# Kernel tuning notes

Measured on AMD Instinct MI355X. Metric: run time of the kernel, lower is better.

## Reference

```python
import jax, jax.numpy as jnp
import numpy as np

B, IN, N, W, R, U, OUT = 512, 128, 256, 64, 4, 256, 128
IFACE = R * W + 3 * W + 5 * R + 3  # 471
CLIP = 20.0
EPS = 1e-6


def setup_inputs() -> dict:
    key = jax.random.key(0)
    ks = jax.random.split(key, 20)
    return {
        'inputs': jax.random.normal(ks[0], (B, IN), jnp.float32),
        'M': jax.random.normal(ks[1], (B, N, W), jnp.float32),
        'usage': jax.random.uniform(ks[2], (B, N), jnp.float32),
        'link': jax.random.uniform(ks[3], (B, N, N), jnp.float32) * 0.01,
        'precedence': jax.random.uniform(ks[4], (B, N), jnp.float32) * 0.01,
        'ww_prev': jax.random.uniform(ks[5], (B, N), jnp.float32) / N,
        'wr_prev': jax.random.uniform(ks[6], (B, N, R), jnp.float32) / N,
        'h_prev': jax.random.normal(ks[7], (B, U), jnp.float32),
        'c_prev': jax.random.normal(ks[8], (B, U), jnp.float32),
        'rv_prev': jax.random.normal(ks[9], (B, W, R), jnp.float32),
        'Wk': jax.random.normal(ks[10], (IN + W * R, 4 * U), jnp.float32) * 0.05,
        'Wr': jax.random.normal(ks[11], (U, 4 * U), jnp.float32) * 0.05,
        'b_lstm': jnp.full((4 * U,), 0.1, jnp.float32),
        'Wi': jax.random.normal(ks[12], (U, IFACE), jnp.float32) * 0.05,
        'bi': jnp.full((IFACE,), 0.1, jnp.float32),
        'Wo': jax.random.normal(ks[13], (U + W * R, OUT), jnp.float32) * 0.05,
        'bo': jnp.zeros((OUT,), jnp.float32),
    }


def _parse_interface(v):
    sizes = [R * W, R, W, 1, W, W, R, 1, 1, 3 * R]
    offs = np.cumsum([0] + sizes)
    s = [v[:, offs[i]:offs[i + 1]] for i in range(len(sizes))]
    read_keys = s[0].reshape(-1, W, R)
    read_strengths = 1.0 + jax.nn.softplus(s[1])                 # [B,R]
    write_key = s[2].reshape(-1, W)                              # [B,W]
    write_strength = 1.0 + jax.nn.softplus(s[3])                 # [B,1]
    erase = jax.nn.sigmoid(s[4])                                 # [B,W]
    write_vec = s[5]                                             # [B,W]
    free_gates = jax.nn.sigmoid(s[6])                            # [B,R]
    alloc_gate = jax.nn.sigmoid(s[7])                            # [B,1]
    write_gate = jax.nn.sigmoid(s[8])                            # [B,1]
    read_modes = jax.nn.softmax(s[9].reshape(-1, 3, R), axis=1)  # [B,3,R]
    return (read_keys, read_strengths, write_key, write_strength, erase,
            write_vec, free_gates, alloc_gate, write_gate, read_modes)


def _forward(inputs, M, usage, link, precedence, ww_prev, wr_prev,
             h_prev, c_prev, rv_prev, Wk, Wr, b_lstm, Wi, bi, Wo, bo):
    # --- controller (keras LSTMCell: gate order i,f,c,o) ---
    x = jnp.concatenate([inputs, rv_prev.reshape(-1, W * R)], axis=1)
    z = x @ Wk + h_prev @ Wr + b_lstm
    zi, zf, zc, zo = jnp.split(z, 4, axis=1)
    c = jax.nn.sigmoid(zf) * c_prev + jax.nn.sigmoid(zi) * jnp.tanh(zc)
    h = jax.nn.sigmoid(zo) * jnp.tanh(c)
    h = jnp.clip(h, -CLIP, CLIP)
    # --- interface ---
    (read_keys, read_strengths, write_key, write_strength, erase,
     write_vec, free_gates, alloc_gate, write_gate, read_modes) = _parse_interface(h @ Wi + bi)
    # --- usage / retention ---
    psi = jnp.prod(1.0 - free_gates[:, None, :] * wr_prev, axis=2)     # [B,N]
    u = (usage + ww_prev - usage * ww_prev) * psi                      # [B,N]
    # --- allocation (sorted cumprod) ---
    idx = jnp.argsort(u, axis=1)                                        # ascending
    u_sorted = jnp.take_along_axis(u, idx, axis=1)
    cp = jnp.cumprod(u_sorted, axis=1)
    cp_excl = jnp.concatenate([jnp.ones_like(cp[:, :1]), cp[:, :-1]], axis=1)
    a_sorted = (1.0 - u_sorted) * cp_excl
    inv = jnp.argsort(idx, axis=1)
    alloc = jnp.take_along_axis(a_sorted, inv, axis=1)                  # [B,N]
    # --- write content addressing (cosine) ---
    Mn = jnp.linalg.norm(M, axis=2)                                     # [B,N]
    kw_n = jnp.linalg.norm(write_key, axis=1, keepdims=True)            # [B,1]
    sim_w = jnp.einsum('bnw,bw->bn', M, write_key) / (Mn * kw_n + EPS)
    cw = jax.nn.softmax(write_strength * sim_w, axis=1)                 # [B,N]
    ww = write_gate * (alloc_gate * alloc + (1.0 - alloc_gate) * cw)    # [B,N]
    # --- memory write ---
    M_new = M * (1.0 - ww[:, :, None] * erase[:, None, :]) + ww[:, :, None] * write_vec[:, None, :]
    # --- temporal link / precedence ---
    L_new = (1.0 - ww[:, :, None] - ww[:, None, :]) * link + ww[:, :, None] * precedence[:, None, :]
    L_new = L_new * (1.0 - jnp.eye(N, dtype=L_new.dtype))
    p_new = (1.0 - jnp.sum(ww, axis=1, keepdims=True)) * precedence + ww
    # --- read content addressing ---
    Mn2 = jnp.linalg.norm(M_new, axis=2)                                # [B,N]
    kr_n = jnp.linalg.norm(read_keys, axis=1)                           # [B,R]
    sim_r = jnp.einsum('bnw,bwr->bnr', M_new, read_keys) / (Mn2[:, :, None] * kr_n[:, None, :] + EPS)
    cr = jax.nn.softmax(read_strengths[:, None, :] * sim_r, axis=1)     # [B,N,R]
    # --- forward / backward weightings ---
    fwd = jnp.einsum('bnm,bmr->bnr', L_new, wr_prev)
    bwd = jnp.einsum('bmn,bmr->bnr', L_new, wr_prev)
    wr = (read_modes[:, 0, :][:, None, :] * bwd
          + read_modes[:, 1, :][:, None, :] * cr
          + read_modes[:, 2, :][:, None, :] * fwd)                      # [B,N,R]
    read_vectors = jnp.einsum('bnw,bnr->bwr', M_new, wr)                # [B,W,R]
    # --- final output ---
    final = jnp.concatenate([h, read_vectors.reshape(-1, W * R)], axis=1) @ Wo + bo
    return jnp.clip(final, -CLIP, CLIP)


def reference(inputs, M, usage, link, precedence, ww_prev, wr_prev,
              h_prev, c_prev, rv_prev, Wk, Wr, b_lstm, Wi, bi, Wo, bo):
    return _forward(inputs, M, usage, link, precedence, ww_prev, wr_prev,
                    h_prev, c_prev, rv_prev, Wk, Wr, b_lstm, Wi, bi, Wo, bo)
```

## Files before the change

### kernel.cpp

```cpp
#include <hip/hip_runtime.h>
#include <math.h>

#define Bsz 512
#define INsz 128
#define Nn 256
#define Ww 64
#define Rr 4
#define Uu 256
#define OUTsz 128
#define IFACEsz 471
#define XDIM 384
#define KL 640
#define G4 1024

__device__ __forceinline__ float sigf(float x){ return 1.0f/(1.0f+expf(-x)); }
__device__ __forceinline__ float softplusf_(float x){ return fmaxf(x,0.0f) + log1pf(expf(-fabsf(x))); }
__device__ __forceinline__ float4 f4fma(float s, float4 a, float4 acc){
  acc.x += s*a.x; acc.y += s*a.y; acc.z += s*a.z; acc.w += s*a.w; return acc;
}
__device__ __forceinline__ float4 f4add(float4 a, float4 b){
  a.x+=b.x; a.y+=b.y; a.z+=b.z; a.w+=b.w; return a;
}
__device__ __forceinline__ float4 f4max(float4 a, float4 b){
  a.x=fmaxf(a.x,b.x); a.y=fmaxf(a.y,b.y); a.z=fmaxf(a.z,b.z); a.w=fmaxf(a.w,b.w); return a;
}

__global__ __launch_bounds__(256) void k_packWi(
  const float* __restrict__ Wi, float* __restrict__ Wip)
{
  const int k = blockIdx.x, t = threadIdx.x;
  const int j2 = t + 256;
  Wip[(size_t)k*512 + t]  = Wi[(size_t)k*IFACEsz + t];
  Wip[(size_t)k*512 + j2] = (j2 < IFACEsz) ? Wi[(size_t)k*IFACEsz + j2] : 0.0f;
}

__global__ __launch_bounds__(512) void k_lstm(
  const float* __restrict__ inputs, const float* __restrict__ rvp,
  const float* __restrict__ hp, const float* __restrict__ Wk,
  const float* __restrict__ Wr, const float* __restrict__ bl,
  const float* __restrict__ cprev, float* __restrict__ h_out)
{
  const int t = threadIdx.x;
  const int tx = t & 7;
  const int tg = (t >> 3) & 3;
  const int tb = t >> 5;
  const int b0 = blockIdx.x * 16;
  const int cg = blockIdx.y * 32;
  const int col = tg*256 + cg + tx*4;
  __shared__ float Xs[16][68];
  __shared__ float zs[16][4][36];
  float4 acc = {0,0,0,0};
  for (int kc = 0; kc < KL; kc += 64){
    if (t < 256){
      const int rr = t >> 4, cc = (t & 15)*4;
      const int c = kc + cc;
      const float* src;
      if (c < INsz)      src = inputs + (size_t)(b0+rr)*INsz + c;
      else if (c < XDIM) src = rvp + (size_t)(b0+rr)*(Ww*Rr) + (c - INsz);
      else               src = hp + (size_t)(b0+rr)*Uu + (c - XDIM);
      *reinterpret_cast<float4*>(&Xs[rr][cc]) = *reinterpret_cast<const float4*>(src);
    }
    __syncthreads();
    const float* Wp = ((kc < XDIM) ? (Wk + (size_t)kc*G4) : (Wr + (size_t)(kc-XDIM)*G4)) + col;
    #pragma unroll 8
    for (int kk=0; kk<64; ++kk){
      float4 w4 = *reinterpret_cast<const float4*>(Wp + (size_t)kk*G4);
      acc = f4fma(Xs[tb][kk], w4, acc);
    }
    __syncthreads();
  }
  {
    float4 b4 = *reinterpret_cast<const float4*>(bl + col);
    acc = f4add(acc, b4);
  }
  *reinterpret_cast<float4*>(&zs[tb][tg][tx*4]) = acc;
  __syncthreads();
  {
    const int b = t >> 5, c = t & 31;
    float zi = zs[b][0][c], zf = zs[b][1][c], zc_ = zs[b][2][c], zo = zs[b][3][c];
    float cc = sigf(zf)*cprev[(size_t)(b0+b)*Uu + cg + c] + sigf(zi)*tanhf(zc_);
    float h = sigf(zo)*tanhf(cc);
    h = fminf(fmaxf(h,-20.0f),20.0f);
    h_out[(size_t)(b0+b)*Uu + cg + c] = h;
  }
}

__global__ __launch_bounds__(256) void k_ifgemm(
  const float* __restrict__ h_ws, const float* __restrict__ Wip, float* __restrict__ v_ws)
{
  const int t = threadIdx.x;
  const int tx = t & 15, ty = t >> 4;
  const int b0 = blockIdx.x*16;
  const int col = blockIdx.y*64 + tx*4;
  __shared__ float Hs[16][68];
  float4 acc = {0,0,0,0};
  for (int kc = 0; kc < Uu; kc += 64){
    {
      int rr = t >> 4, cc = (t & 15)*4;
      *reinterpret_cast<float4*>(&Hs[rr][cc]) =
        *reinterpret_cast<const float4*>(h_ws + (size_t)(b0+rr)*Uu + kc + cc);
    }
    __syncthreads();
    const float* Wp = Wip + (size_t)kc*512 + col;
    #pragma unroll 8
    for (int kk=0; kk<64; ++kk){
      float4 w4 = *reinterpret_cast<const float4*>(Wp + (size_t)kk*512);
      acc = f4fma(Hs[ty][kk], w4, acc);
    }
    __syncthreads();
  }
  *reinterpret_cast<float4*>(v_ws + (size_t)(b0+ty)*512 + col) = acc;
}

__global__ __launch_bounds__(256) void k_iface2(
  const float* __restrict__ v_ws, const float* __restrict__ bi,
  const float* __restrict__ usage, const float* __restrict__ wwp,
  const float* __restrict__ wrp, const float* __restrict__ prec,
  const float* __restrict__ M,
  float* __restrict__ ww_ws, float* __restrict__ er_ws, float* __restrict__ wv_ws,
  float* __restrict__ rk_ws, float* __restrict__ krn_ws, float* __restrict__ rstr_ws,
  float* __restrict__ rm_ws, float* __restrict__ P_ws, float* __restrict__ Q_ws)
{
  const int b = blockIdx.x, t = threadIdx.x;
  __shared__ float vl[IFACEsz];
  __shared__ float wkey[Ww];
  __shared__ float ul[Nn], sul[Nn], cpl[Nn], red[Nn];
  __shared__ __align__(16) float4 red4[Nn];
  __shared__ float scal[8];
  for (int j=t; j<IFACEsz; j+=256) vl[j] = v_ws[(size_t)b*512 + j] + bi[j];
  __syncthreads();
  if (t < Ww){
    wkey[t] = vl[260+t];
    er_ws[b*Ww+t] = sigf(vl[325+t]);
    wv_ws[b*Ww+t] = vl[389+t];
  }
  rk_ws[b*Ww*Rr + t] = vl[t];
  if (t < Rr){
    rstr_ws[b*Rr+t] = 1.0f + softplusf_(vl[256+t]);
    float ssum = 0.0f;
    for (int w=0;w<Ww;++w){ float v = vl[w*Rr+t]; ssum += v*v; }
    krn_ws[b*Rr+t] = sqrtf(ssum);
    float q0=vl[459+t], q1=vl[463+t], q2=vl[467+t];
    float mm = fmaxf(q0, fmaxf(q1,q2));
    float e0=expf(q0-mm), e1=expf(q1-mm), e2=expf(q2-mm);
    float inv = 1.0f/(e0+e1+e2);
    rm_ws[b*12 + t]     = e0*inv;
    rm_ws[b*12 + 4 + t] = e1*inv;
    rm_ws[b*12 + 8 + t] = e2*inv;
    scal[4+t] = sigf(vl[453+t]);
  }
  if (t == 0){
    scal[0] = 1.0f + softplusf_(vl[324]);
    scal[1] = sigf(vl[457]);
    scal[2] = sigf(vl[458]);
    float ssum=0.0f;
    for (int w=0;w<Ww;++w){ float v=vl[260+w]; ssum += v*v; }
    scal[3] = sqrtf(ssum);
  }
  __syncthreads();
  float4 wr4 = *reinterpret_cast<const float4*>(wrp + ((size_t)b*Nn + t)*Rr);
  float psi = (1.0f - scal[4]*wr4.x)*(1.0f - scal[5]*wr4.y)
            * (1.0f - scal[6]*wr4.z)*(1.0f - scal[7]*wr4.w);
  float us = usage[b*Nn+t], wp = wwp[b*Nn+t];
  float u = (us + wp - us*wp)*psi;
  ul[t] = u;
  __syncthreads();
  int rank = 0;
  for (int m=0;m<Nn;++m){
    float um = ul[m];
    rank += (um < u || (um == u && m < t)) ? 1 : 0;
  }
  sul[rank] = u;
  __syncthreads();
  cpl[t] = sul[t];
  __syncthreads();
  for (int d=1; d<Nn; d<<=1){
    float a = cpl[t];
    float m_ = (t >= d) ? cpl[t-d] : 1.0f;
    __syncthreads();
    cpl[t] = a*m_;
    __syncthreads();
  }
  float cpexcl = (rank == 0) ? 1.0f : cpl[rank-1];
  float alloc = (1.0f - u)*cpexcl;
  const float* Mrow = M + ((size_t)b*Nn + t)*Ww;
  float dot=0.0f, nrm=0.0f;
  #pragma unroll 4
  for (int w=0;w<Ww;w+=4){
    float4 m4 = *reinterpret_cast<const float4*>(Mrow + w);
    dot += m4.x*wkey[w] + m4.y*wkey[w+1] + m4.z*wkey[w+2] + m4.w*wkey[w+3];
    nrm += m4.x*m4.x + m4.y*m4.y + m4.z*m4.z + m4.w*m4.w;
  }
  float sim = dot/(sqrtf(nrm)*scal[3] + 1e-6f);
  float sc = scal[0]*sim;
  red[t] = sc; __syncthreads();
  for (int st=128; st>0; st>>=1){ if (t<st) red[t] = fmaxf(red[t], red[t+st]); __syncthreads(); }
  float mx = red[0]; __syncthreads();
  float e = expf(sc - mx);
  red[t] = e; __syncthreads();
  for (int st=128; st>0; st>>=1){ if (t<st) red[t] += red[t+st]; __syncthreads(); }
  float cw = e/red[0];
  float ww = scal[2]*(scal[1]*alloc + (1.0f - scal[1])*cw);
  ww_ws[b*Nn+t] = ww;
  __syncthreads();
  float pr = prec[b*Nn+t];
  float4 pv; pv.x = pr*wr4.x; pv.y = pr*wr4.y; pv.z = pr*wr4.z; pv.w = pr*wr4.w;
  red4[t] = pv; __syncthreads();
  for (int st=128; st>0; st>>=1){ if (t<st) red4[t] = f4add(red4[t], red4[t+st]); __syncthreads(); }
  if (t==0) *reinterpret_cast<float4*>(P_ws + b*Rr) = red4[0];
  __syncthreads();
  float4 qv; qv.x = ww*wr4.x; qv.y = ww*wr4.y; qv.z = ww*wr4.z; qv.w = ww*wr4.w;
  red4[t] = qv; __syncthreads();
  for (int st=128; st>0; st>>=1){ if (t<st) red4[t] = f4add(red4[t], red4[t+st]); __syncthreads(); }
  if (t==0) *reinterpret_cast<float4*>(Q_ws + b*Rr) = red4[0];
}

__global__ __launch_bounds__(256) void k_link(
  const float* __restrict__ link, const float* __restrict__ wrp,
  const float* __restrict__ ww_ws,
  float* __restrict__ rowA, float* __restrict__ rowC,
  float* __restrict__ colAp, float* __restrict__ colCp, float* __restrict__ diag)
{
  const int b = blockIdx.x, s = blockIdx.y, t = threadIdx.x;
  const int n0 = s*64;
  __shared__ __align__(16) float4 wrl4[Nn];
  __shared__ __align__(16) float wws[Nn];
  wrl4[t] = *reinterpret_cast<const float4*>(wrp + ((size_t)b*Nn + t)*Rr);
  wws[t]  = ww_ws[(size_t)b*Nn + t];
  __syncthreads();
  const float* Lb = link + (size_t)b*Nn*Nn;
  {
    float4 cA = {0,0,0,0}, cC = {0,0,0,0};
    float dg = 0.0f;
    #pragma unroll 4
    for (int i=0;i<64;++i){
      const int n = n0 + i;
      float l = Lb[(size_t)n*Nn + t];
      float4 wn = wrl4[n];
      cA = f4fma(l, wn, cA);
      cC = f4fma(l*wws[n], wn, cC);
      if (n == t) dg = l;
    }
    *reinterpret_cast<float4*>(colAp + (((size_t)s*Bsz + b)*Nn + t)*Rr) = cA;
    *reinterpret_cast<float4*>(colCp + (((size_t)s*Bsz + b)*Nn + t)*Rr) = cC;
    if (t >= n0 && t < n0+64) diag[(size_t)b*Nn + t] = dg;
  }
  {
    const int row = n0 + (t >> 2), seg = t & 3;
    const float* Lr = Lb + (size_t)row*Nn + seg*64;
    float ra0=0,ra1=0,ra2=0,ra3=0, rc0=0,rc1=0,rc2=0,rc3=0;
    #pragma unroll
    for (int k=0;k<16;++k){
      float4 l4 = *reinterpret_cast<const float4*>(Lr + k*4);
      const int m0 = seg*64 + k*4;
      float4 ww4 = *reinterpret_cast<const float4*>(&wws[m0]);
      float4 w0 = wrl4[m0], w1 = wrl4[m0+1], w2 = wrl4[m0+2], w3 = wrl4[m0+3];
      ra0 += l4.x*w0.x + l4.y*w1.x + l4.z*w2.x + l4.w*w3.x;
      ra1 += l4.x*w0.y + l4.y*w1.y + l4.z*w2.y + l4.w*w3.y;
      ra2 += l4.x*w0.z + l4.y*w1.z + l4.z*w2.z + l4.w*w3.z;
      ra3 += l4.x*w0.w + l4.y*w1.w + l4.z*w2.w + l4.w*w3.w;
      float lx=l4.x*ww4.x, ly=l4.y*ww4.y, lz=l4.z*ww4.z, lw=l4.w*ww4.w;
      rc0 += lx*w0.x + ly*w1.x + lz*w2.x + lw*w3.x;
      rc1 += lx*w0.y + ly*w1.y + lz*w2.y + lw*w3.y;
      rc2 += lx*w0.z + ly*w1.z + lz*w2.z + lw*w3.z;
      rc3 += lx*w0.w + ly*w1.w + lz*w2.w + lw*w3.w;
    }
    #pragma unroll
    for (int off=2; off>=1; off>>=1){
      ra0 += __shfl_down(ra0, off, 4); ra1 += __shfl_down(ra1, off, 4);
      ra2 += __shfl_down(ra2, off, 4); ra3 += __shfl_down(ra3, off, 4);
      rc0 += __shfl_down(rc0, off, 4); rc1 += __shfl_down(rc1, off, 4);
      rc2 += __shfl_down(rc2, off, 4); rc3 += __shfl_down(rc3, off, 4);
    }
    if (seg == 0){
      float4 oA; oA.x=ra0; oA.y=ra1; oA.z=ra2; oA.w=ra3;
      float4 oC; oC.x=rc0; oC.y=rc1; oC.z=rc2; oC.w=rc3;
      *reinterpret_cast<float4*>(rowA + ((size_t)b*Nn + row)*Rr) = oA;
      *reinterpret_cast<float4*>(rowC + ((size_t)b*Nn + row)*Rr) = oC;
    }
  }
}

__global__ __launch_bounds__(256) void k_readw_rv(
  const float* __restrict__ M, const float* __restrict__ ww_ws,
  const float* __restrict__ er_ws, const float* __restrict__ wv_ws,
  const float* __restrict__ rk_ws, const float* __restrict__ krn_ws,
  const float* __restrict__ rstr_ws, const float* __restrict__ rm_ws,
  const float* __restrict__ P_ws, const float* __restrict__ Q_ws,
  const float* __restrict__ rowA, const float* __restrict__ rowC,
  const float* __restrict__ colAp, const float* __restrict__ colCp,
  const float* __restrict__ diag, const float* __restrict__ wrp,
  const float* __restrict__ prec, float* __restrict__ rv_ws)
{
  const int b = blockIdx.x, t = threadIdx.x;
  __shared__ float rkl[Ww*Rr];
  __shared__ float erl[Ww], wvl[Ww];
  __shared__ __align__(16) float4 red4[Nn];
  __shared__ float wrl[Nn][4];
  __shared__ float wwl[Nn];
  rkl[t] = rk_ws[b*Ww*Rr + t];
  if (t < Ww){ erl[t] = er_ws[b*Ww+t]; wvl[t] = wv_ws[b*Ww+t]; }
  const float ww = ww_ws[b*Nn+t];
  wwl[t] = ww;
  __syncthreads();
  const float pr = prec[b*Nn+t];
  const float dg = diag[b*Nn+t];
  float4 wr4 = *reinterpret_cast<const float4*>(wrp + ((size_t)b*Nn+t)*Rr);
  const float Lnn = (1.0f - 2.0f*ww)*dg + ww*pr;
  float4 rA = *reinterpret_cast<const float4*>(rowA + ((size_t)b*Nn+t)*Rr);
  float4 rC = *reinterpret_cast<const float4*>(rowC + ((size_t)b*Nn+t)*Rr);
  float4 cA = {0,0,0,0}, cC = {0,0,0,0};
  #pragma unroll
  for (int sp=0; sp<4; ++sp){
    cA = f4add(cA, *reinterpret_cast<const float4*>(colAp + (((size_t)sp*Bsz + b)*Nn + t)*Rr));
    cC = f4add(cC, *reinterpret_cast<const float4*>(colCp + (((size_t)sp*Bsz + b)*Nn + t)*Rr));
  }
  float4 Pv = *reinterpret_cast<const float4*>(P_ws + b*Rr);
  float4 Qv = *reinterpret_cast<const float4*>(Q_ws + b*Rr);
  float fwdv[4], bwdv[4];
  fwdv[0] = (1.0f-ww)*rA.x - rC.x + ww*Pv.x - Lnn*wr4.x;
  fwdv[1] = (1.0f-ww)*rA.y - rC.y + ww*Pv.y - Lnn*wr4.y;
  fwdv[2] = (1.0f-ww)*rA.z - rC.z + ww*Pv.z - Lnn*wr4.z;
  fwdv[3] = (1.0f-ww)*rA.w - rC.w + ww*Pv.w - Lnn*wr4.w;
  bwdv[0] = (1.0f-ww)*cA.x - cC.x + pr*Qv.x - Lnn*wr4.x;
  bwdv[1] = (1.0f-ww)*cA.y - cC.y + pr*Qv.y - Lnn*wr4.y;
  bwdv[2] = (1.0f-ww)*cA.z - cC.z + pr*Qv.z - Lnn*wr4.z;
  bwdv[3] = (1.0f-ww)*cA.w - cC.w + pr*Qv.w - Lnn*wr4.w;
  const float* Mrow = M + ((size_t)b*Nn + t)*Ww;
  float s0=0,s1=0,s2=0,s3=0, nrm=0;
  #pragma unroll 4
  for (int w=0;w<Ww;w+=4){
    float4 m4 = *reinterpret_cast<const float4*>(Mrow + w);
    float mvs[4] = {m4.x, m4.y, m4.z, m4.w};
    #pragma unroll
    for (int i=0;i<4;++i){
      int w_ = w+i;
      float mn = mvs[i]*(1.0f - ww*erl[w_]) + ww*wvl[w_];
      nrm += mn*mn;
      float4 k4 = *reinterpret_cast<const float4*>(&rkl[w_*4]);
      s0 += mn*k4.x; s1 += mn*k4.y; s2 += mn*k4.z; s3 += mn*k4.w;
    }
  }
  float mnorm = sqrtf(nrm);
  float4 kn = *reinterpret_cast<const float4*>(krn_ws + b*Rr);
  float4 rs = *reinterpret_cast<const float4*>(rstr_ws + b*Rr);
  float4 aa4;
  aa4.x = rs.x*(s0/(mnorm*kn.x + 1e-6f));
  aa4.y = rs.y*(s1/(mnorm*kn.y + 1e-6f));
  aa4.z = rs.z*(s2/(mnorm*kn.z + 1e-6f));
  aa4.w = rs.w*(s3/(mnorm*kn.w + 1e-6f));
  red4[t] = aa4; __syncthreads();
  for (int st=128; st>0; st>>=1){ if (t<st) red4[t] = f4max(red4[t], red4[t+st]); __syncthreads(); }
  float4 mx4 = red4[0]; __syncthreads();
  float4 e4;
  e4.x = expf(aa4.x - mx4.x); e4.y = expf(aa4.y - mx4.y);
  e4.z = expf(aa4.z - mx4.z); e4.w = expf(aa4.w - mx4.w);
  red4[t] = e4; __syncthreads();
  for (int st=128; st>0; st>>=1){ if (t<st) red4[t] = f4add(red4[t], red4[t+st]); __syncthreads(); }
  float4 sm4 = red4[0];
  float cr[4] = {e4.x/sm4.x, e4.y/sm4.y, e4.z/sm4.z, e4.w/sm4.w};
  float wro[4];
  #pragma unroll
  for (int r=0;r<4;++r){
    float m0 = rm_ws[b*12 + r];
    float m1 = rm_ws[b*12 + 4 + r];
    float m2 = rm_ws[b*12 + 8 + r];
    wro[r] = m0*bwdv[r] + m1*cr[r] + m2*fwdv[r];
  }
  wrl[t][0]=wro[0]; wrl[t][1]=wro[1]; wrl[t][2]=wro[2]; wrl[t][3]=wro[3];
  __syncthreads();
  {
    const int w = t & 63, r = t >> 6;
    const float er_w = erl[w], wv_w = wvl[w];
    float a0=0.0f, a1=0.0f, a2=0.0f, a3=0.0f;
    for (int n=0;n<Nn;n+=4){
      float m0v = M[((size_t)b*Nn + n  )*Ww + w];
      float m1v = M[((size_t)b*Nn + n+1)*Ww + w];
      float m2v = M[((size_t)b*Nn + n+2)*Ww + w];
      float m3v = M[((size_t)b*Nn + n+3)*Ww + w];
      float w0 = wwl[n], w1 = wwl[n+1], w2 = wwl[n+2], w3 = wwl[n+3];
      a0 += (m0v*(1.0f - w0*er_w) + w0*wv_w)*wrl[n  ][r];
      a1 += (m1v*(1.0f - w1*er_w) + w1*wv_w)*wrl[n+1][r];
      a2 += (m2v*(1.0f - w2*er_w) + w2*wv_w)*wrl[n+2][r];
      a3 += (m3v*(1.0f - w3*er_w) + w3*wv_w)*wrl[n+3][r];
    }
    rv_ws[(size_t)b*(Ww*Rr) + w*Rr + r] = (a0+a1)+(a2+a3);
  }
}

__global__ __launch_bounds__(256) void k_final(
  const float* __restrict__ h_ws, const float* __restrict__ rv_ws,
  const float* __restrict__ Wo, const float* __restrict__ bo,
  float* __restrict__ out)
{
  const int t = threadIdx.x;
  const int tx = t & 15, ty = t >> 4;
  const int b0 = blockIdx.x*16;
  const int col = blockIdx.y*64 + tx*4;
  __shared__ float Cs[16][68];
  float4 acc = {0,0,0,0};
  for (int kc = 0; kc < 512; kc += 64){
    {
      int rr = t >> 4, cc = (t & 15)*4;
      const float* src = (kc < Uu)
        ? (h_ws  + (size_t)(b0+rr)*Uu + kc + cc)
        : (rv_ws + (size_t)(b0+rr)*(Ww*Rr) + (kc-Uu) + cc);
      *reinterpret_cast<float4*>(&Cs[rr][cc]) = *reinterpret_cast<const float4*>(src);
    }
    __syncthreads();
    const float* Wp = Wo + (size_t)kc*OUTsz + col;
    #pragma unroll 8
    for (int kk=0; kk<64; ++kk){
      float4 w4 = *reinterpret_cast<const float4*>(Wp + (size_t)kk*OUTsz);
      acc = f4fma(Cs[ty][kk], w4, acc);
    }
    __syncthreads();
  }
  float4 b4 = *reinterpret_cast<const float4*>(bo + col);
  acc.x = fminf(fmaxf(acc.x + b4.x, -20.0f), 20.0f);
  acc.y = fminf(fmaxf(acc.y + b4.y, -20.0f), 20.0f);
  acc.z = fminf(fmaxf(acc.z + b4.z, -20.0f), 20.0f);
  acc.w = fminf(fmaxf(acc.w + b4.w, -20.0f), 20.0f);
  *reinterpret_cast<float4*>(out + (size_t)(b0+ty)*OUTsz + col) = acc;
}

extern "C" void kernel_launch(void* const* d_in, const int* in_sizes, int n_in,
                              void* d_out, int out_size, void* d_ws, size_t ws_size,
                              hipStream_t stream)
{
  const float* inputs = (const float*)d_in[0];
  const float* M      = (const float*)d_in[1];
  const float* usage  = (const float*)d_in[2];
  const float* link   = (const float*)d_in[3];
  const float* prec   = (const float*)d_in[4];
  const float* wwp    = (const float*)d_in[5];
  const float* wrp    = (const float*)d_in[6];
  const float* hp     = (const float*)d_in[7];
  const float* cp     = (const float*)d_in[8];
  const float* rvp    = (const float*)d_in[9];
  const float* Wk     = (const float*)d_in[10];
  const float* Wr     = (const float*)d_in[11];
  const float* bl     = (const float*)d_in[12];
  const float* Wi     = (const float*)d_in[13];
  const float* bi     = (const float*)d_in[14];
  const float* Wo     = (const float*)d_in[15];
  const float* bo     = (const float*)d_in[16];

  float* ws = (float*)d_ws;
  float* Wip     = ws;
  float* v_ws    = Wip    + (size_t)Uu*512;
  float* h_ws    = v_ws   + (size_t)Bsz*512;
  float* ww_ws   = h_ws   + (size_t)Bsz*Uu;
  float* er_ws   = ww_ws  + (size_t)Bsz*Nn;
  float* wv_ws   = er_ws  + (size_t)Bsz*Ww;
  float* rk_ws   = wv_ws  + (size_t)Bsz*Ww;
  float* krn_ws  = rk_ws  + (size_t)Bsz*Ww*Rr;
  float* rstr_ws = krn_ws + (size_t)Bsz*Rr;
  float* rm_ws   = rstr_ws+ (size_t)Bsz*Rr;
  float* P_ws    = rm_ws  + (size_t)Bsz*3*Rr;
  float* Q_ws    = P_ws   + (size_t)Bsz*Rr;
  float* rowA    = Q_ws   + (size_t)Bsz*Rr;
  float* rowC    = rowA   + (size_t)Bsz*Nn*Rr;
  float* colAp   = rowC   + (size_t)Bsz*Nn*Rr;
  float* colCp   = colAp  + (size_t)4*Bsz*Nn*Rr;
  float* diag    = colCp  + (size_t)4*Bsz*Nn*Rr;
  float* rv_ws   = diag   + (size_t)Bsz*Nn;

  k_packWi<<<dim3(Uu), dim3(256), 0, stream>>>(Wi, Wip);
  k_lstm<<<dim3(32,8), dim3(512), 0, stream>>>(inputs, rvp, hp, Wk, Wr, bl, cp, h_ws);
  k_ifgemm<<<dim3(32,8), dim3(256), 0, stream>>>(h_ws, Wip, v_ws);
  k_iface2<<<dim3(Bsz), dim3(256), 0, stream>>>(v_ws, bi, usage, wwp, wrp, prec, M,
      ww_ws, er_ws, wv_ws, rk_ws, krn_ws, rstr_ws, rm_ws, P_ws, Q_ws);
  k_link<<<dim3(Bsz,4), dim3(256), 0, stream>>>(link, wrp, ww_ws, rowA, rowC, colAp, colCp, diag);
  k_readw_rv<<<dim3(Bsz), dim3(256), 0, stream>>>(M, ww_ws, er_ws, wv_ws, rk_ws, krn_ws,
      rstr_ws, rm_ws, P_ws, Q_ws, rowA, rowC, colAp, colCp, diag, wrp, prec, rv_ws);
  k_final<<<dim3(32,2), dim3(256), 0, stream>>>(h_ws, rv_ws, Wo, bo, (float*)d_out);
}
```

Before: 188.4 us.

## Vectorize link column pass with float4 loads and padded LDS for row pass

The column-reduction pass of k_link now has each thread load float4 of four adjacent columns over 16 rows, with four row-groups whose partial sums are combined through a shared-memory reduction. Each thread previously read one float per row. The row pass now reads read/write weights from padded per-segment LDS copies to avoid bank conflicts. The goal is fewer, wider global loads on the link matrix and less LDS conflict, at the cost of more registers, extra syncs and about 16KB more LDS, which may lower occupancy.

```diff
diff --git a/kernel.cpp b/kernel.cpp
--- a/kernel.cpp
+++ b/kernel.cpp
@@ -224,26 +224,54 @@
   const int b = blockIdx.x, s = blockIdx.y, t = threadIdx.x;
   const int n0 = s*64;
   __shared__ __align__(16) float4 wrl4[Nn];
-  __shared__ __align__(16) float wws[Nn];
-  wrl4[t] = *reinterpret_cast<const float4*>(wrp + ((size_t)b*Nn + t)*Rr);
-  wws[t]  = ww_ws[(size_t)b*Nn + t];
+  __shared__ __align__(16) float4 wrl4p[4][66];
+  __shared__ float wws[Nn];
+  __shared__ float wwsp[4][68];
+  __shared__ __align__(16) float4 cred[4][Nn];
+  {
+    float4 w4 = *reinterpret_cast<const float4*>(wrp + ((size_t)b*Nn + t)*Rr);
+    wrl4[t] = w4;
+    wrl4p[t>>6][t&63] = w4;
+    float w = ww_ws[(size_t)b*Nn + t];
+    wws[t] = w;
+    wwsp[t>>6][t&63] = w;
+  }
   __syncthreads();
   const float* Lb = link + (size_t)b*Nn*Nn;
+  const int cq = t & 63, g = t >> 6;
+  const int c4 = cq*4;
   {
-    float4 cA = {0,0,0,0}, cC = {0,0,0,0};
-    float dg = 0.0f;
-    #pragma unroll 4
-    for (int i=0;i<64;++i){
-      const int n = n0 + i;
-      float l = Lb[(size_t)n*Nn + t];
+    float4 z = {0,0,0,0};
+    float4 a0=z,a1=z,a2=z,a3=z, q0=z,q1=z,q2=z,q3=z;
+    #pragma unroll
+    for (int i=0;i<16;++i){
+      const int n = n0 + g*16 + i;
+      float4 l4 = *reinterpret_cast<const float4*>(Lb + (size_t)n*Nn + c4);
       float4 wn = wrl4[n];
-      cA = f4fma(l, wn, cA);
-      cC = f4fma(l*wws[n], wn, cC);
-      if (n == t) dg = l;
-    }
-    *reinterpret_cast<float4*>(colAp + (((size_t)s*Bsz + b)*Nn + t)*Rr) = cA;
-    *reinterpret_cast<float4*>(colCp + (((size_t)s*Bsz + b)*Nn + t)*Rr) = cC;
-    if (t >= n0 && t < n0+64) diag[(size_t)b*Nn + t] = dg;
+      float wwn = wws[n];
+      a0 = f4fma(l4.x, wn, a0); a1 = f4fma(l4.y, wn, a1);
+      a2 = f4fma(l4.z, wn, a2); a3 = f4fma(l4.w, wn, a3);
+      q0 = f4fma(l4.x*wwn, wn, q0); q1 = f4fma(l4.y*wwn, wn, q1);
+      q2 = f4fma(l4.z*wwn, wn, q2); q3 = f4fma(l4.w*wwn, wn, q3);
+      if ((n>>2) == cq){
+        const int r = n&3;
+        float c = (r==0) ? l4.x : (r==1) ? l4.y : (r==2) ? l4.z : l4.w;
+        diag[(size_t)b*Nn + n] = c;
+      }
+    }
+    cred[g][c4+0]=a0; cred[g][c4+1]=a1; cred[g][c4+2]=a2; cred[g][c4+3]=a3;
+    __syncthreads();
+    {
+      float4 sA = f4add(f4add(cred[0][t],cred[1][t]),f4add(cred[2][t],cred[3][t]));
+      *reinterpret_cast<float4*>(colAp + (((size_t)s*Bsz + b)*Nn + t)*Rr) = sA;
+    }
+    __syncthreads();
+    cred[g][c4+0]=q0; cred[g][c4+1]=q1; cred[g][c4+2]=q2; cred[g][c4+3]=q3;
+    __syncthreads();
+    {
+      float4 sC = f4add(f4add(cred[0][t],cred[1][t]),f4add(cred[2][t],cred[3][t]));
+      *reinterpret_cast<float4*>(colCp + (((size_t)s*Bsz + b)*Nn + t)*Rr) = sC;
+    }
   }
   {
     const int row = n0 + (t >> 2), seg = t & 3;
@@ -252,9 +280,9 @@
     #pragma unroll
     for (int k=0;k<16;++k){
       float4 l4 = *reinterpret_cast<const float4*>(Lr + k*4);
-      const int m0 = seg*64 + k*4;
-      float4 ww4 = *reinterpret_cast<const float4*>(&wws[m0]);
-      float4 w0 = wrl4[m0], w1 = wrl4[m0+1], w2 = wrl4[m0+2], w3 = wrl4[m0+3];
+      float4 ww4 = *reinterpret_cast<const float4*>(&wwsp[seg][k*4]);
+      float4 w0 = wrl4p[seg][k*4], w1 = wrl4p[seg][k*4+1];
+      float4 w2 = wrl4p[seg][k*4+2], w3 = wrl4p[seg][k*4+3];
       ra0 += l4.x*w0.x + l4.y*w1.x + l4.z*w2.x + l4.w*w3.x;
       ra1 += l4.x*w0.y + l4.y*w1.y + l4.z*w2.y + l4.w*w3.y;
       ra2 += l4.x*w0.z + l4.y*w1.z + l4.z*w2.z + l4.w*w3.z;
```

Measured after the change: 188.9 us. No clear change (+0.3%).

## Split link kernel into separate column and row reduction blocks with batched loads

Applied to the files above, without the earlier changes.

Doubles the link kernel grid so that column-sum and row-sum work over each 64-row slab run in different blocks, not sequentially in the same block. The column path now has each thread load a float4 across 16 rows up front and reduce four partial groups through shared memory. The row path preloads all 16 float4s before computing and uses padded shared-memory layouts to reduce bank conflicts. The aim is more memory-level parallelism and occupancy on the dominant 128MB link read. The cost is more blocks, extra shared-memory reductions and higher register pressure from the preload arrays.

```diff
diff --git a/kernel.cpp b/kernel.cpp
--- a/kernel.cpp
+++ b/kernel.cpp
@@ -24,6 +24,7 @@
 __device__ __forceinline__ float4 f4max(float4 a, float4 b){
   a.x=fmaxf(a.x,b.x); a.y=fmaxf(a.y,b.y); a.z=fmaxf(a.z,b.z); a.w=fmaxf(a.w,b.w); return a;
 }
+__device__ __forceinline__ float4 L4(const float* p){ return *reinterpret_cast<const float4*>(p); }
 
 __global__ __launch_bounds__(256) void k_packWi(
   const float* __restrict__ Wi, float* __restrict__ Wip)
@@ -221,40 +222,75 @@
   float* __restrict__ rowA, float* __restrict__ rowC,
   float* __restrict__ colAp, float* __restrict__ colCp, float* __restrict__ diag)
 {
-  const int b = blockIdx.x, s = blockIdx.y, t = threadIdx.x;
-  const int n0 = s*64;
-  __shared__ __align__(16) float4 wrl4[Nn];
-  __shared__ __align__(16) float wws[Nn];
-  wrl4[t] = *reinterpret_cast<const float4*>(wrp + ((size_t)b*Nn + t)*Rr);
-  wws[t]  = ww_ws[(size_t)b*Nn + t];
-  __syncthreads();
+  const int b = blockIdx.x, role = blockIdx.y, t = threadIdx.x;
+  __shared__ __align__(16) char smem[21504];
   const float* Lb = link + (size_t)b*Nn*Nn;
-  {
-    float4 cA = {0,0,0,0}, cC = {0,0,0,0};
-    float dg = 0.0f;
-    #pragma unroll 4
-    for (int i=0;i<64;++i){
-      const int n = n0 + i;
-      float l = Lb[(size_t)n*Nn + t];
-      float4 wn = wrl4[n];
-      cA = f4fma(l, wn, cA);
-      cC = f4fma(l*wws[n], wn, cC);
-      if (n == t) dg = l;
-    }
-    *reinterpret_cast<float4*>(colAp + (((size_t)s*Bsz + b)*Nn + t)*Rr) = cA;
-    *reinterpret_cast<float4*>(colCp + (((size_t)s*Bsz + b)*Nn + t)*Rr) = cC;
-    if (t >= n0 && t < n0+64) diag[(size_t)b*Nn + t] = dg;
-  }
-  {
+  if (role < 4){
+    const int s = role, n0 = s*64;
+    float4* wrl4 = reinterpret_cast<float4*>(smem);
+    float*  wws  = reinterpret_cast<float*>(smem + 4096);
+    float4* cred = reinterpret_cast<float4*>(smem + 5120);
+    wrl4[t] = L4(wrp + ((size_t)b*Nn + t)*Rr);
+    wws[t]  = ww_ws[(size_t)b*Nn + t];
+    __syncthreads();
+    const int cq = t & 63, g = t >> 6, c4 = cq*4;
+    const float* pa = Lb + (size_t)(n0 + g*16)*Nn + c4;
+    float4 rr[16];
+    #pragma unroll
+    for (int j=0;j<16;++j) rr[j] = L4(pa + (size_t)j*Nn);
+    float4 z = {0,0,0,0};
+    float4 aA0=z,aA1=z,aA2=z,aA3=z, aQ0=z,aQ1=z,aQ2=z,aQ3=z;
+    #pragma unroll
+    for (int j=0;j<16;++j){
+      const int n = n0 + g*16 + j;
+      float4 wn = wrl4[n]; float wwn = wws[n];
+      aA0=f4fma(rr[j].x,wn,aA0); aA1=f4fma(rr[j].y,wn,aA1);
+      aA2=f4fma(rr[j].z,wn,aA2); aA3=f4fma(rr[j].w,wn,aA3);
+      aQ0=f4fma(rr[j].x*wwn,wn,aQ0); aQ1=f4fma(rr[j].y*wwn,wn,aQ1);
+      aQ2=f4fma(rr[j].z*wwn,wn,aQ2); aQ3=f4fma(rr[j].w*wwn,wn,aQ3);
+    }
+    cred[g*Nn + c4+0]=aA0; cred[g*Nn + c4+1]=aA1;
+    cred[g*Nn + c4+2]=aA2; cred[g*Nn + c4+3]=aA3;
+    __syncthreads();
+    {
+      float4 sA = f4add(f4add(cred[t],cred[Nn+t]),f4add(cred[2*Nn+t],cred[3*Nn+t]));
+      *reinterpret_cast<float4*>(colAp + (((size_t)s*Bsz + b)*Nn + t)*Rr) = sA;
+    }
+    __syncthreads();
+    cred[g*Nn + c4+0]=aQ0; cred[g*Nn + c4+1]=aQ1;
+    cred[g*Nn + c4+2]=aQ2; cred[g*Nn + c4+3]=aQ3;
+    __syncthreads();
+    {
+      float4 sC = f4add(f4add(cred[t],cred[Nn+t]),f4add(cred[2*Nn+t],cred[3*Nn+t]));
+      *reinterpret_cast<float4*>(colCp + (((size_t)s*Bsz + b)*Nn + t)*Rr) = sC;
+    }
+    if (t < 64){
+      const int n = n0 + t;
+      diag[(size_t)b*Nn + n] = Lb[(size_t)n*Nn + n];
+    }
+  } else {
+    const int s = role - 4, n0 = s*64;
+    float4* wrl4p = reinterpret_cast<float4*>(smem);
+    float*  wwsp  = reinterpret_cast<float*>(smem + 4224);
+    {
+      float4 w4 = L4(wrp + ((size_t)b*Nn + t)*Rr);
+      wrl4p[(t>>6)*66 + (t&63)] = w4;
+      wwsp[(t>>6)*68 + (t&63)]  = ww_ws[(size_t)b*Nn + t];
+    }
+    __syncthreads();
     const int row = n0 + (t >> 2), seg = t & 3;
     const float* Lr = Lb + (size_t)row*Nn + seg*64;
+    float4 rr[16];
+    #pragma unroll
+    for (int j=0;j<16;++j) rr[j] = L4(Lr + j*4);
     float ra0=0,ra1=0,ra2=0,ra3=0, rc0=0,rc1=0,rc2=0,rc3=0;
     #pragma unroll
-    for (int k=0;k<16;++k){
-      float4 l4 = *reinterpret_cast<const float4*>(Lr + k*4);
-      const int m0 = seg*64 + k*4;
-      float4 ww4 = *reinterpret_cast<const float4*>(&wws[m0]);
-      float4 w0 = wrl4[m0], w1 = wrl4[m0+1], w2 = wrl4[m0+2], w3 = wrl4[m0+3];
+    for (int j=0;j<16;++j){
+      const int j0 = j*4;
+      float4 l4 = rr[j];
+      float4 ww4 = *reinterpret_cast<const float4*>(&wwsp[seg*68 + j0]);
+      float4 w0 = wrl4p[seg*66 + j0],   w1 = wrl4p[seg*66 + j0+1];
+      float4 w2 = wrl4p[seg*66 + j0+2], w3 = wrl4p[seg*66 + j0+3];
       ra0 += l4.x*w0.x + l4.y*w1.x + l4.z*w2.x + l4.w*w3.x;
       ra1 += l4.x*w0.y + l4.y*w1.y + l4.z*w2.y + l4.w*w3.y;
       ra2 += l4.x*w0.z + l4.y*w1.z + l4.z*w2.z + l4.w*w3.z;
@@ -471,7 +507,7 @@
   k_ifgemm<<<dim3(32,8), dim3(256), 0, stream>>>(h_ws, Wip, v_ws);
   k_iface2<<<dim3(Bsz), dim3(256), 0, stream>>>(v_ws, bi, usage, wwp, wrp, prec, M,
       ww_ws, er_ws, wv_ws, rk_ws, krn_ws, rstr_ws, rm_ws, P_ws, Q_ws);
-  k_link<<<dim3(Bsz,4), dim3(256), 0, stream>>>(link, wrp, ww_ws, rowA, rowC, colAp, colCp, diag);
+  k_link<<<dim3(Bsz,8), dim3(256), 0, stream>>>(link, wrp, ww_ws, rowA, rowC, colAp, colCp, diag);
   k_readw_rv<<<dim3(Bsz), dim3(256), 0, stream>>>(M, ww_ws, er_ws, wv_ws, rk_ws, krn_ws,
       rstr_ws, rm_ws, P_ws, Q_ws, rowA, rowC, colAp, colCp, diag, wrp, prec, rv_ws);
   k_final<<<dim3(32,2), dim3(256), 0, stream>>>(h_ws, rv_ws, Wo, bo, (float*)d_out);
```

New measurement: 186.3 us. No clear change (-1.1%).

## Stage link tiles in LDS to share one global read between row and column passes

Applied to the files above, without the earlier changes.

The link kernel used to read each 64-row slab of the link matrix from global memory twice, once for the column (forward) sums and once for the row (backward) sums. It now loads 16-row chunks into a padded shared-memory tile with float4 loads and computes both sums, plus the diagonal, from that tile. This roughly halves global traffic on the largest input (128 MB of link data). The cost is extra LDS use, two barriers per chunk and a 16-lane shuffle reduction for the row sums.

```diff
diff --git a/kernel.cpp b/kernel.cpp
--- a/kernel.cpp
+++ b/kernel.cpp
@@ -24,6 +24,7 @@
 __device__ __forceinline__ float4 f4max(float4 a, float4 b){
   a.x=fmaxf(a.x,b.x); a.y=fmaxf(a.y,b.y); a.z=fmaxf(a.z,b.z); a.w=fmaxf(a.w,b.w); return a;
 }
+__device__ __forceinline__ float4 L4(const float* p){ return *reinterpret_cast<const float4*>(p); }
 
 __global__ __launch_bounds__(256) void k_packWi(
   const float* __restrict__ Wi, float* __restrict__ Wip)
@@ -224,61 +225,70 @@
   const int b = blockIdx.x, s = blockIdx.y, t = threadIdx.x;
   const int n0 = s*64;
   __shared__ __align__(16) float4 wrl4[Nn];
-  __shared__ __align__(16) float wws[Nn];
-  wrl4[t] = *reinterpret_cast<const float4*>(wrp + ((size_t)b*Nn + t)*Rr);
-  wws[t]  = ww_ws[(size_t)b*Nn + t];
+  __shared__ float wrs[4][Nn];
+  __shared__ float wws[Nn];
+  __shared__ float Ls[16][264];
+  {
+    float4 w4 = L4(wrp + ((size_t)b*Nn + t)*Rr);
+    wrl4[t] = w4;
+    wrs[0][t]=w4.x; wrs[1][t]=w4.y; wrs[2][t]=w4.z; wrs[3][t]=w4.w;
+    wws[t] = ww_ws[(size_t)b*Nn + t];
+  }
   __syncthreads();
   const float* Lb = link + (size_t)b*Nn*Nn;
-  {
-    float4 cA = {0,0,0,0}, cC = {0,0,0,0};
-    float dg = 0.0f;
-    #pragma unroll 4
-    for (int i=0;i<64;++i){
-      const int n = n0 + i;
-      float l = Lb[(size_t)n*Nn + t];
+  float4 cA = {0,0,0,0}, cC = {0,0,0,0};
+  const int rr = t >> 4, li = t & 15;
+  #pragma unroll
+  for (int ch = 0; ch < 4; ++ch){
+    const int base = n0 + ch*16;
+    #pragma unroll
+    for (int j=0;j<4;++j){
+      const int idx = j*256 + t;
+      const int r_ = idx >> 6, c4_ = (idx & 63)*4;
+      float4 v = L4(Lb + (size_t)(base + r_)*Nn + c4_);
+      *reinterpret_cast<float4*>(&Ls[r_][c4_]) = v;
+    }
+    __syncthreads();
+    #pragma unroll
+    for (int i=0;i<16;++i){
+      const int n = base + i;
+      float l = Ls[i][t];
       float4 wn = wrl4[n];
       cA = f4fma(l, wn, cA);
       cC = f4fma(l*wws[n], wn, cC);
-      if (n == t) dg = l;
-    }
-    *reinterpret_cast<float4*>(colAp + (((size_t)s*Bsz + b)*Nn + t)*Rr) = cA;
-    *reinterpret_cast<float4*>(colCp + (((size_t)s*Bsz + b)*Nn + t)*Rr) = cC;
-    if (t >= n0 && t < n0+64) diag[(size_t)b*Nn + t] = dg;
-  }
-  {
-    const int row = n0 + (t >> 2), seg = t & 3;
-    const float* Lr = Lb + (size_t)row*Nn + seg*64;
-    float ra0=0,ra1=0,ra2=0,ra3=0, rc0=0,rc1=0,rc2=0,rc3=0;
-    #pragma unroll
-    for (int k=0;k<16;++k){
-      float4 l4 = *reinterpret_cast<const float4*>(Lr + k*4);
-      const int m0 = seg*64 + k*4;
-      float4 ww4 = *reinterpret_cast<const float4*>(&wws[m0]);
-      float4 w0 = wrl4[m0], w1 = wrl4[m0+1], w2 = wrl4[m0+2], w3 = wrl4[m0+3];
-      ra0 += l4.x*w0.x + l4.y*w1.x + l4.z*w2.x + l4.w*w3.x;
-      ra1 += l4.x*w0.y + l4.y*w1.y + l4.z*w2.y + l4.w*w3.y;
-      ra2 += l4.x*w0.z + l4.y*w1.z + l4.z*w2.z + l4.w*w3.z;
-      ra3 += l4.x*w0.w + l4.y*w1.w + l4.z*w2.w + l4.w*w3.w;
-      float lx=l4.x*ww4.x, ly=l4.y*ww4.y, lz=l4.z*ww4.z, lw=l4.w*ww4.w;
-      rc0 += lx*w0.x + ly*w1.x + lz*w2.x + lw*w3.x;
-      rc1 += lx*w0.y + ly*w1.y + lz*w2.y + lw*w3.y;
-      rc2 += lx*w0.z + ly*w1.z + lz*w2.z + lw*w3.z;
-      rc3 += lx*w0.w + ly*w1.w + lz*w2.w + lw*w3.w;
-    }
-    #pragma unroll
-    for (int off=2; off>=1; off>>=1){
-      ra0 += __shfl_down(ra0, off, 4); ra1 += __shfl_down(ra1, off, 4);
-      ra2 += __shfl_down(ra2, off, 4); ra3 += __shfl_down(ra3, off, 4);
-      rc0 += __shfl_down(rc0, off, 4); rc1 += __shfl_down(rc1, off, 4);
-      rc2 += __shfl_down(rc2, off, 4); rc3 += __shfl_down(rc3, off, 4);
-    }
-    if (seg == 0){
-      float4 oA; oA.x=ra0; oA.y=ra1; oA.z=ra2; oA.w=ra3;
-      float4 oC; oC.x=rc0; oC.y=rc1; oC.z=rc2; oC.w=rc3;
-      *reinterpret_cast<float4*>(rowA + ((size_t)b*Nn + row)*Rr) = oA;
-      *reinterpret_cast<float4*>(rowC + ((size_t)b*Nn + row)*Rr) = oC;
-    }
-  }
+    }
+    if (t >= base && t < base+16){
+      diag[(size_t)b*Nn + t] = Ls[t - base][t];
+    }
+    {
+      float pa0=0,pa1=0,pa2=0,pa3=0, pc0=0,pc1=0,pc2=0,pc3=0;
+      #pragma unroll
+      for (int k=0;k<16;++k){
+        const int c = li + k*16;
+        float l = Ls[rr][c];
+        float w0 = wrs[0][c], w1 = wrs[1][c], w2 = wrs[2][c], w3 = wrs[3][c];
+        float lw = l * wws[c];
+        pa0 += l*w0;  pa1 += l*w1;  pa2 += l*w2;  pa3 += l*w3;
+        pc0 += lw*w0; pc1 += lw*w1; pc2 += lw*w2; pc3 += lw*w3;
+      }
+      #pragma unroll
+      for (int off=8; off>=1; off>>=1){
+        pa0 += __shfl_down(pa0, off, 16); pa1 += __shfl_down(pa1, off, 16);
+        pa2 += __shfl_down(pa2, off, 16); pa3 += __shfl_down(pa3, off, 16);
+        pc0 += __shfl_down(pc0, off, 16); pc1 += __shfl_down(pc1, off, 16);
+        pc2 += __shfl_down(pc2, off, 16); pc3 += __shfl_down(pc3, off, 16);
+      }
+      if (li == 0){
+        float4 oA; oA.x=pa0; oA.y=pa1; oA.z=pa2; oA.w=pa3;
+        float4 oC; oC.x=pc0; oC.y=pc1; oC.z=pc2; oC.w=pc3;
+        *reinterpret_cast<float4*>(rowA + ((size_t)b*Nn + base + rr)*Rr) = oA;
+        *reinterpret_cast<float4*>(rowC + ((size_t)b*Nn + base + rr)*Rr) = oC;
+      }
+    }
+    __syncthreads();
+  }
+  *reinterpret_cast<float4*>(colAp + (((size_t)s*Bsz + b)*Nn + t)*Rr) = cA;
+  *reinterpret_cast<float4*>(colCp + (((size_t)s*Bsz + b)*Nn + t)*Rr) = cC;
 }
 
 __global__ __launch_bounds__(256) void k_readw_rv(
```

Measured after the change: 206.9 us. 1.1x slower.
